# Kernel optimization log

Measured on AMD Instinct MI355X. Metric: run time of the kernel, lower is better.

Reference implementation:

```python
import jax, jax.numpy as jnp
import numpy as np

B, N_PER = 1048576, 32
MAX_COUNT = 5  # counts >= 5 lumped into the '>4' bucket (severity 3)


def setup_inputs() -> dict:
    key = jax.random.key(0)
    k1, k2, k3 = jax.random.split(key, 3)
    x1 = jax.random.uniform(k1, (B, N_PER), dtype=jnp.float32)
    x2 = jax.random.uniform(k2, (B, N_PER), dtype=jnp.float32)
    x3 = jax.random.uniform(k3, (B, N_PER), dtype=jnp.float32)
    return {"x1": x1, "x2": x2, "x3": x3}


def _count_distribution(p):
    # p: [B, N] independent fact probabilities.
    # Poisson-binomial DP over facts with count capped at MAX_COUNT (absorbing).
    b = p.shape[0]
    init = jnp.zeros((b, MAX_COUNT + 1), p.dtype).at[:, 0].set(1.0)

    def step(c, pi):
        pi = pi[:, None]                              # [B,1]
        shifted = jnp.pad(c[:, :-1], ((0, 0), (1, 0)))  # count+1
        new = c * (1.0 - pi) + shifted * pi
        # absorbing top bucket: staying in >=MAX_COUNT regardless of pi
        new = new.at[:, -1].add(c[:, -1] * pi[:, 0])
        return new, None

    counts, _ = jax.lax.scan(step, init, p.T)  # scan over facts axis
    return counts  # [B, MAX_COUNT+1]


def reference(x1, x2, x3):
    p = jnp.concatenate([x1, x2, x3], axis=1)  # [B, 96]
    c = _count_distribution(p)
    # severity(0): n==0; severity(1): 1<=n<=2; severity(2): 3<=n<=4;
    # severity(3): n>4; severity(4): never derivable -> 0
    sev = jnp.stack(
        [c[:, 0], c[:, 1] + c[:, 2], c[:, 3] + c[:, 4], c[:, 5],
         jnp.zeros_like(c[:, 0])],
        axis=1,
    )
    return sev  # [B, 5]
```

## Files before the change

### kernel.cpp

```cpp
#include <hip/hip_runtime.h>


#define ROWS_PER_BLOCK 128
#define THREADS 128

__global__ __launch_bounds__(THREADS) void hemorrhage_kernel(
    const float* __restrict__ x1,
    const float* __restrict__ x2,
    const float* __restrict__ x3,
    float* __restrict__ out)
{
    __shared__ float smem[3 * ROWS_PER_BLOCK * 32];

    const int t = threadIdx.x;
    const int l = t & 63;
    const int w = t >> 6;
    const long long block_row0 = (long long)blockIdx.x * ROWS_PER_BLOCK;

    const int lrow8 = l >> 3;
    const int lcol  = (l & 7) ^ (lrow8 & 7);

    const float* srcs[3] = {x1, x2, x3};
#pragma unroll
    for (int a = 0; a < 3; ++a) {
        const float* src = srcs[a];
#pragma unroll
        for (int i = 0; i < 8; ++i) {
            const int rlocal = i * 16 + w * 8 + lrow8;
            const float* gptr = src + (block_row0 + rlocal) * 32 + lcol * 4;
            float* lptr = &smem[a * (ROWS_PER_BLOCK * 32) + (i * 16 + w * 8) * 32];
            __builtin_amdgcn_global_load_lds(
                (const __attribute__((address_space(1))) void*)gptr,
                (__attribute__((address_space(3))) void*)lptr,
                16, 0, 0);
        }
    }
    __syncthreads();

    float c0 = 1.0f, c1 = 0.0f, c2 = 0.0f, c3 = 0.0f, c4 = 0.0f, c5 = 0.0f;
    const int tswz = t & 7;
#pragma unroll
    for (int a = 0; a < 3; ++a) {
        const float4* rowbase =
            (const float4*)&smem[a * (ROWS_PER_BLOCK * 32) + t * 32];
#pragma unroll
        for (int j = 0; j < 8; ++j) {
            const float4 p4 = rowbase[j ^ tswz];
            const float ps[4] = {p4.x, p4.y, p4.z, p4.w};
#pragma unroll
            for (int k = 0; k < 4; ++k) {
                const float p = ps[k];
                const float q = 1.0f - p;
                c5 = fmaf(c4, p, c5);
                c4 = fmaf(c4, q, c3 * p);
                c3 = fmaf(c3, q, c2 * p);
                c2 = fmaf(c2, q, c1 * p);
                c1 = fmaf(c1, q, c0 * p);
                c0 = c0 * q;
            }
        }
    }

    __syncthreads();
    smem[t * 5 + 0] = c0;
    smem[t * 5 + 1] = c1 + c2;
    smem[t * 5 + 2] = c3 + c4;
    smem[t * 5 + 3] = c5;
    smem[t * 5 + 4] = 0.0f;
    __syncthreads();

    float* outb = out + block_row0 * 5;
#pragma unroll
    for (int k = 0; k < 5; ++k) {
        outb[k * THREADS + t] = smem[k * THREADS + t];
    }
}

extern "C" void kernel_launch(void* const* d_in, const int* in_sizes, int n_in,
                              void* d_out, int out_size, void* d_ws, size_t ws_size,
                              hipStream_t stream) {
    const float* x1 = (const float*)d_in[0];
    const float* x2 = (const float*)d_in[1];
    const float* x3 = (const float*)d_in[2];
    float* out = (float*)d_out;

    const int rows = in_sizes[0] / 32;
    const int blocks = rows / ROWS_PER_BLOCK;
    hemorrhage_kernel<<<blocks, THREADS, 0, stream>>>(x1, x2, x3, out);
}
```

Baseline: 357.6 us.

## Split each row across 8 lanes and merge partial count distributions via shuffles

Replaces the one-thread-per-row design, which staged loads through LDS, with eight lanes per row. Each lane reads one float4 from each input directly from global memory, runs the capped DP over its 12 probabilities, and the lanes combine their partial distributions with a butterfly of xor-shuffles using truncated convolution. The top bucket is recovered as one minus the sum of the lower buckets. This removes LDS staging and barriers and makes the serial dependency chain much shorter, at the cost of extra shuffle and convolution work and a possible rounding difference in the top bucket.

```diff
diff --git a/kernel.cpp b/kernel.cpp
--- a/kernel.cpp
+++ b/kernel.cpp
@@ -1,78 +1,81 @@
 #include <hip/hip_runtime.h>
 
 
-#define ROWS_PER_BLOCK 128
-#define THREADS 128
+#define THREADS 256
 
-__global__ __launch_bounds__(THREADS) void hemorrhage_kernel(
+__global__ __launch_bounds__(THREADS, 6) void hemorrhage_kernel(
     const float* __restrict__ x1,
     const float* __restrict__ x2,
     const float* __restrict__ x3,
     float* __restrict__ out)
 {
-    __shared__ float smem[3 * ROWS_PER_BLOCK * 32];
+    const int t = threadIdx.x;
+    const int m = t & 7;
+    const int row = blockIdx.x * (THREADS / 8) + (t >> 3);
+    const size_t base = (size_t)row * 32 + (size_t)m * 4;
 
-    const int t = threadIdx.x;
-    const int l = t & 63;
-    const int w = t >> 6;
-    const long long block_row0 = (long long)blockIdx.x * ROWS_PER_BLOCK;
+    const float4 p1 = *(const float4*)(x1 + base);
+    const float4 p2 = *(const float4*)(x2 + base);
+    const float4 p3 = *(const float4*)(x3 + base);
 
-    const int lrow8 = l >> 3;
-    const int lcol  = (l & 7) ^ (lrow8 & 7);
+    float a0 = 1.0f, a1 = 0.0f, a2 = 0.0f, a3 = 0.0f, a4 = 0.0f, a5 = 0.0f;
 
-    const float* srcs[3] = {x1, x2, x3};
+#define STEP(P)                          \
+    do {                                 \
+        const float p_ = (P);            \
+        const float q_ = 1.0f - p_;      \
+        a5 = fmaf(a4, p_, a5);           \
+        a4 = fmaf(a4, q_, a3 * p_);      \
+        a3 = fmaf(a3, q_, a2 * p_);      \
+        a2 = fmaf(a2, q_, a1 * p_);      \
+        a1 = fmaf(a1, q_, a0 * p_);      \
+        a0 = a0 * q_;                    \
+    } while (0)
+
+    STEP(p1.x); STEP(p1.y); STEP(p1.z); STEP(p1.w);
+    STEP(p2.x); STEP(p2.y); STEP(p2.z); STEP(p2.w);
+    STEP(p3.x); STEP(p3.y); STEP(p3.z); STEP(p3.w);
+#undef STEP
+
 #pragma unroll
-    for (int a = 0; a < 3; ++a) {
-        const float* src = srcs[a];
-#pragma unroll
-        for (int i = 0; i < 8; ++i) {
-            const int rlocal = i * 16 + w * 8 + lrow8;
-            const float* gptr = src + (block_row0 + rlocal) * 32 + lcol * 4;
-            float* lptr = &smem[a * (ROWS_PER_BLOCK * 32) + (i * 16 + w * 8) * 32];
-            __builtin_amdgcn_global_load_lds(
-                (const __attribute__((address_space(1))) void*)gptr,
-                (__attribute__((address_space(3))) void*)lptr,
-                16, 0, 0);
-        }
-    }
-    __syncthreads();
+    for (int d = 1; d < 8; d <<= 1) {
+        const float b0 = __shfl_xor(a0, d);
+        const float b1 = __shfl_xor(a1, d);
+        const float b2 = __shfl_xor(a2, d);
+        const float b3 = __shfl_xor(a3, d);
+        const float b4 = __shfl_xor(a4, d);
+        const float b5 = __shfl_xor(a5, d);
 
-    float c0 = 1.0f, c1 = 0.0f, c2 = 0.0f, c3 = 0.0f, c4 = 0.0f, c5 = 0.0f;
-    const int tswz = t & 7;
-#pragma unroll
-    for (int a = 0; a < 3; ++a) {
-        const float4* rowbase =
-            (const float4*)&smem[a * (ROWS_PER_BLOCK * 32) + t * 32];
-#pragma unroll
-        for (int j = 0; j < 8; ++j) {
-            const float4 p4 = rowbase[j ^ tswz];
-            const float ps[4] = {p4.x, p4.y, p4.z, p4.w};
-#pragma unroll
-            for (int k = 0; k < 4; ++k) {
-                const float p = ps[k];
-                const float q = 1.0f - p;
-                c5 = fmaf(c4, p, c5);
-                c4 = fmaf(c4, q, c3 * p);
-                c3 = fmaf(c3, q, c2 * p);
-                c2 = fmaf(c2, q, c1 * p);
-                c1 = fmaf(c1, q, c0 * p);
-                c0 = c0 * q;
-            }
-        }
+        float n0 = a0 * b0;
+        float n1 = a0 * b1;
+        n1 = fmaf(a1, b0, n1);
+        float n2 = a0 * b2;
+        n2 = fmaf(a1, b1, n2);
+        n2 = fmaf(a2, b0, n2);
+        float n3 = a0 * b3;
+        n3 = fmaf(a1, b2, n3);
+        n3 = fmaf(a2, b1, n3);
+        n3 = fmaf(a3, b0, n3);
+        float n4 = a0 * b4;
+        n4 = fmaf(a1, b3, n4);
+        n4 = fmaf(a2, b2, n4);
+        n4 = fmaf(a3, b1, n4);
+        n4 = fmaf(a4, b0, n4);
+        const float n5 = 1.0f - (((n0 + n1) + (n2 + n3)) + n4);
+
+        a0 = n0; a1 = n1; a2 = n2; a3 = n3; a4 = n4; a5 = n5;
     }
 
-    __syncthreads();
-    smem[t * 5 + 0] = c0;
-    smem[t * 5 + 1] = c1 + c2;
-    smem[t * 5 + 2] = c3 + c4;
-    smem[t * 5 + 3] = c5;
-    smem[t * 5 + 4] = 0.0f;
-    __syncthreads();
-
-    float* outb = out + block_row0 * 5;
-#pragma unroll
-    for (int k = 0; k < 5; ++k) {
-        outb[k * THREADS + t] = smem[k * THREADS + t];
+    if (m < 5) {
+        float v;
+        switch (m) {
+            case 0: v = a0; break;
+            case 1: v = a1 + a2; break;
+            case 2: v = a3 + a4; break;
+            case 3: v = a5; break;
+            default: v = 0.0f; break;
+        }
+        out[(size_t)row * 5 + m] = v;
     }
 }
 
@@ -85,6 +88,6 @@
     float* out = (float*)d_out;
 
     const int rows = in_sizes[0] / 32;
-    const int blocks = rows / ROWS_PER_BLOCK;
+    const int blocks = rows / (THREADS / 8);
     hemorrhage_kernel<<<blocks, THREADS, 0, stream>>>(x1, x2, x3, out);
 }
```

Measured after the change: 346.6 us. 1.03x faster.
